# Kernel optimization log

Hardware: AMD Instinct MI355X
Metric: run time of the kernel (lower is better)

## Reference

```python
import jax, jax.numpy as jnp
import numpy as np

P = 4096      # particles per event
F = 128       # max features per particle (inner ragged axis)
H = 128       # hidden_size


def setup_inputs() -> dict:
    key = jax.random.key(0)
    ks = jax.random.split(key, 12)
    s = 1.0 / np.sqrt(H)  # torch RNN default init scale
    u = lambda k, shp: jax.random.uniform(k, shp, jnp.float32, -s, s)
    event = jax.random.normal(ks[0], (P, F, 1), jnp.float32)
    lengths = jnp.maximum(1, jax.random.randint(ks[1], (P,), 0, F))  # ragged lengths in [1, F)
    return {
        "event": event,
        "lengths": lengths,
        "W_ih1": u(ks[2], (H, 1)), "W_hh1": u(ks[3], (H, H)),
        "b_ih1": u(ks[4], (H,)),   "b_hh1": u(ks[5], (H,)),
        "W_ih2": u(ks[6], (H, H)), "W_hh2": u(ks[7], (H, H)),
        "b_ih2": u(ks[8], (H,)),   "b_hh2": u(ks[9], (H,)),
    }


def reference(event, lengths, W_ih1, W_hh1, b_ih1, b_hh1,
              W_ih2, W_hh2, b_ih2, b_hh2):
    # net1: vanilla tanh RNN over each particle's feature sequence (batched over P).
    # Ragged lengths handled by masking the hidden-state update past each length.
    Pn, Fn, _ = event.shape
    mask = jnp.arange(Fn)[:, None] < lengths[None, :]      # [F, P]
    xs = jnp.transpose(event, (1, 0, 2))                   # [F, P, 1] time-major

    def step1(h, xm):
        x, m = xm                                          # x:[P,1], m:[P]
        h_new = jnp.tanh(x @ W_ih1.T + b_ih1 + h @ W_hh1.T + b_hh1)
        return jnp.where(m[:, None], h_new, h), None

    h0 = jnp.zeros((Pn, H), event.dtype)
    h1, _ = jax.lax.scan(step1, h0, (xs, mask))            # final hidden per particle: [P, H]

    # net2: tanh RNN over the sequence of particle hidden states (unbatched).
    def step2(h, x):
        return jnp.tanh(x @ W_ih2.T + b_ih2 + h @ W_hh2.T + b_hh2), None

    h2, _ = jax.lax.scan(step2, jnp.zeros((H,), event.dtype), h1)
    return h2[None, :]                                     # torch hidden shape (1, H)
```

## Files before the change

kernel.cpp:

```cpp
#include <hip/hip_runtime.h>


constexpr int PN = 4096;
constexpr int FN = 128;
constexpr int HN = 128;
constexpr int CH  = 64;
constexpr int NCH = PN / CH;

__device__ __forceinline__ float fast_tanh(float x) {
    float e = __expf(2.0f * x);
    return 1.0f - 2.0f / (e + 1.0f);
}

__device__ __forceinline__ void lds_barrier() {
    asm volatile("s_waitcnt lgkmcnt(0)\n\ts_barrier" ::: "memory");
}

__device__ __forceinline__ float dpp_xor1(float x) {
    return __int_as_float(__builtin_amdgcn_update_dpp(
        0, __float_as_int(x), 0xB1 , 0xF, 0xF, true));
}
__device__ __forceinline__ float dpp_xor2(float x) {
    return __int_as_float(__builtin_amdgcn_update_dpp(
        0, __float_as_int(x), 0x4E , 0xF, 0xF, true));
}
__device__ __forceinline__ float dpp_xor4(float x, bool hi) {
    int a = __builtin_amdgcn_update_dpp(0, __float_as_int(x), 0x104, 0xF, 0xF, true);
    int b = __builtin_amdgcn_update_dpp(0, __float_as_int(x), 0x114, 0xF, 0xF, true);
    return __int_as_float(hi ? b : a);
}
__device__ __forceinline__ float dpp_xor8(float x, bool hi) {
    int a = __builtin_amdgcn_update_dpp(0, __float_as_int(x), 0x108, 0xF, 0xF, true);
    int b = __builtin_amdgcn_update_dpp(0, __float_as_int(x), 0x118, 0xF, 0xF, true);
    return __int_as_float(hi ? b : a);
}

__device__ __forceinline__ float reduce16(const float s[8], int jg) {
    const bool hi8 = (jg & 8) != 0;
    float m0 = hi8 ? s[0] : s[4], k0 = hi8 ? s[4] : s[0];
    float m1 = hi8 ? s[1] : s[5], k1 = hi8 ? s[5] : s[1];
    float m2 = hi8 ? s[2] : s[6], k2 = hi8 ? s[6] : s[2];
    float m3 = hi8 ? s[3] : s[7], k3 = hi8 ? s[7] : s[3];
    float x0 = k0 + dpp_xor8(m0, hi8);
    float x1 = k1 + dpp_xor8(m1, hi8);
    float x2 = k2 + dpp_xor8(m2, hi8);
    float x3 = k3 + dpp_xor8(m3, hi8);
    const bool hi4 = (jg & 4) != 0;
    float y0 = (hi4 ? x2 : x0) + dpp_xor4(hi4 ? x0 : x2, hi4);
    float y1 = (hi4 ? x3 : x1) + dpp_xor4(hi4 ? x1 : x3, hi4);
    const bool hi2 = (jg & 2) != 0;
    float z  = (hi2 ? y1 : y0) + dpp_xor2(hi2 ? y0 : y1);
    z += dpp_xor1(z);
    return z;
}
__device__ __forceinline__ int reduce16_cidx(int jg) {
    return ((jg >> 3) & 1) * 4 + ((jg >> 2) & 1) * 2 + ((jg >> 1) & 1);
}

__global__ __launch_bounds__(256) void net1_kernel(
    const float* __restrict__ event,
    const int*   __restrict__ lengths,
    const float* __restrict__ W_ih1,
    const float* __restrict__ W_hh1,
    const float* __restrict__ b_ih1,
    const float* __restrict__ b_hh1,
    const float* __restrict__ W_ih2,
    const float* __restrict__ b_ih2,
    const float* __restrict__ b_hh2,
    float* __restrict__ U)
{
    const int p    = blockIdx.x;
    const int tid  = threadIdx.x;
    const int wv   = tid >> 6;
    const int lane = tid & 63;
    const int jg   = lane & 15;
    const int og16 = (wv << 2) + (lane >> 4);
    const int rot  = (jg >> 2) & 1;
    const int oi_w = og16 * 8 + reduce16_cidx(jg);

    __shared__ float h[2][HN];
    __shared__ float ev[FN];

    if (tid < FN) ev[tid]   = event[p * FN + tid];
    if (tid < HN) h[0][tid] = 0.0f;

    float w[8][8];
    #pragma unroll
    for (int c = 0; c < 8; ++c) {
        const float* row = W_hh1 + (og16 * 8 + c) * HN + jg * 8;
        #pragma unroll
        for (int t = 0; t < 2; ++t) {
            const int krot = (t + rot) & 1;
            float4 v = *reinterpret_cast<const float4*>(row + 4 * krot);
            w[c][4*t+0] = v.x; w[c][4*t+1] = v.y;
            w[c][4*t+2] = v.z; w[c][4*t+3] = v.w;
        }
    }
    const float wx_own   = W_ih1[oi_w];
    const float bias_own = b_ih1[oi_w] + b_hh1[oi_w];
    const int   len      = lengths[p];

    __syncthreads();

    for (int t = 0; t < len; ++t) {
        const int cur = t & 1;
        const float x = ev[t];

        const float* base = &h[cur][jg * 8];
        float s[8] = {0,0,0,0,0,0,0,0};
        #pragma unroll
        for (int tt = 0; tt < 2; ++tt) {
            const int krot = (tt + rot) & 1;
            float4 hv = *reinterpret_cast<const float4*>(base + 4 * krot);
            #pragma unroll
            for (int c = 0; c < 8; ++c) {
                s[c] = fmaf(w[c][4*tt+0], hv.x, s[c]);
                s[c] = fmaf(w[c][4*tt+1], hv.y, s[c]);
                s[c] = fmaf(w[c][4*tt+2], hv.z, s[c]);
                s[c] = fmaf(w[c][4*tt+3], hv.w, s[c]);
            }
        }
        const float z  = reduce16(s, jg);
        const float hn = fast_tanh(z + fmaf(wx_own, x, bias_own));
        if ((jg & 1) == 0) h[cur ^ 1][oi_w] = hn;
        lds_barrier();
    }

    if (tid < HN) {
        const float4* h4 = reinterpret_cast<const float4*>(h[len & 1]);
        const float4* w2 = reinterpret_cast<const float4*>(W_ih2 + tid * HN);
        float a0 = b_ih2[tid] + b_hh2[tid], a1 = 0.f, a2 = 0.f, a3 = 0.f;
        #pragma unroll
        for (int k = 0; k < HN / 4; ++k) {
            float4 hv = h4[k];
            float4 wv = w2[k];
            a0 = fmaf(wv.x, hv.x, a0);
            a1 = fmaf(wv.y, hv.y, a1);
            a2 = fmaf(wv.z, hv.z, a2);
            a3 = fmaf(wv.w, hv.w, a3);
        }
        U[p * HN + tid] = (a0 + a1) + (a2 + a3);
    }
}

__global__ __launch_bounds__(256) void net2_kernel(
    const float* __restrict__ U,
    const float* __restrict__ W_hh2,
    float* __restrict__ out)
{
    const int tid  = threadIdx.x;
    const int wv   = tid >> 6;
    const int lane = tid & 63;
    const int jg   = lane & 15;
    const int og16 = (wv << 2) + (lane >> 4);
    const int rot  = (jg >> 2) & 1;
    const int oi_w = og16 * 8 + reduce16_cidx(jg);

    __shared__ float h[2][HN];
    __shared__ float Ulds[2][CH * HN];

    float w[8][8];
    #pragma unroll
    for (int c = 0; c < 8; ++c) {
        const float* row = W_hh2 + (og16 * 8 + c) * HN + jg * 8;
        #pragma unroll
        for (int t = 0; t < 2; ++t) {
            const int krot = (t + rot) & 1;
            float4 v = *reinterpret_cast<const float4*>(row + 4 * krot);
            w[c][4*t+0] = v.x; w[c][4*t+1] = v.y;
            w[c][4*t+2] = v.z; w[c][4*t+3] = v.w;
        }
    }

    {
        const float4* g = reinterpret_cast<const float4*>(U);
        float4*       l = reinterpret_cast<float4*>(&Ulds[0][0]);
        #pragma unroll
        for (int r = 0; r < 8; ++r) l[r * 256 + tid] = g[r * 256 + tid];
    }
    if (tid < HN) h[0][tid] = 0.0f;
    __syncthreads();

    int buf = 0;
    for (int c = 0; c < NCH; ++c) {
        const int nb = buf ^ 1;

        float4 st[8];
        const int cg = (c + 1 < NCH) ? (c + 1) : c;
        {
            const float4* gsrc = reinterpret_cast<const float4*>(U + cg * CH * HN);
            #pragma unroll
            for (int r = 0; r < 8; ++r) st[r] = gsrc[r * 256 + tid];
        }

        for (int s2 = 0; s2 < CH; ++s2) {
            const int hc = s2 & 1;
            const float u_cur = Ulds[buf][s2 * HN + oi_w];

            const float* base = &h[hc][jg * 8];
            float s[8] = {0,0,0,0,0,0,0,0};
            #pragma unroll
            for (int tt = 0; tt < 2; ++tt) {
                const int krot = (tt + rot) & 1;
                float4 hv = *reinterpret_cast<const float4*>(base + 4 * krot);
                #pragma unroll
                for (int cc = 0; cc < 8; ++cc) {
                    s[cc] = fmaf(w[cc][4*tt+0], hv.x, s[cc]);
                    s[cc] = fmaf(w[cc][4*tt+1], hv.y, s[cc]);
                    s[cc] = fmaf(w[cc][4*tt+2], hv.z, s[cc]);
                    s[cc] = fmaf(w[cc][4*tt+3], hv.w, s[cc]);
                }
            }
            const float z  = reduce16(s, jg);
            const float hn = fast_tanh(z + u_cur);
            if ((jg & 1) == 0) h[hc ^ 1][oi_w] = hn;
            lds_barrier();
        }

        {
            float4* ldst = reinterpret_cast<float4*>(&Ulds[nb][0]);
            #pragma unroll
            for (int r = 0; r < 8; ++r) ldst[r * 256 + tid] = st[r];
        }
        __syncthreads();
        buf = nb;
    }

    if (tid < HN) out[tid] = h[0][tid];
}

extern "C" void kernel_launch(void* const* d_in, const int* in_sizes, int n_in,
                              void* d_out, int out_size, void* d_ws, size_t ws_size,
                              hipStream_t stream)
{
    const float* event   = (const float*)d_in[0];
    const int*   lengths = (const int*)  d_in[1];
    const float* W_ih1   = (const float*)d_in[2];
    const float* W_hh1   = (const float*)d_in[3];
    const float* b_ih1   = (const float*)d_in[4];
    const float* b_hh1   = (const float*)d_in[5];
    const float* W_ih2   = (const float*)d_in[6];
    const float* W_hh2   = (const float*)d_in[7];
    const float* b_ih2   = (const float*)d_in[8];
    const float* b_hh2   = (const float*)d_in[9];
    float* out = (float*)d_out;
    float* U   = (float*)d_ws;

    hipLaunchKernelGGL(net1_kernel, dim3(PN), dim3(256), 0, stream,
                       event, lengths, W_ih1, W_hh1, b_ih1, b_hh1,
                       W_ih2, b_ih2, b_hh2, U);
    hipLaunchKernelGGL(net2_kernel, dim3(1), dim3(256), 0, stream,
                       U, W_hh2, out);
}
```

Measured before the change: 1.875 ms.

## Add per-chunk readiness counters and shorten net2 reduction to 8-lane groups

```diff
diff --git a/kernel.cpp b/kernel.cpp
--- a/kernel.cpp
+++ b/kernel.cpp
@@ -18,11 +18,11 @@
 
 __device__ __forceinline__ float dpp_xor1(float x) {
     return __int_as_float(__builtin_amdgcn_update_dpp(
-        0, __float_as_int(x), 0xB1 , 0xF, 0xF, true));
+        0, __float_as_int(x), 0xB1, 0xF, 0xF, true));
 }
 __device__ __forceinline__ float dpp_xor2(float x) {
     return __int_as_float(__builtin_amdgcn_update_dpp(
-        0, __float_as_int(x), 0x4E , 0xF, 0xF, true));
+        0, __float_as_int(x), 0x4E, 0xF, 0xF, true));
 }
 __device__ __forceinline__ float dpp_xor4(float x, bool hi) {
     int a = __builtin_amdgcn_update_dpp(0, __float_as_int(x), 0x104, 0xF, 0xF, true);
@@ -57,6 +57,7 @@
     return ((jg >> 3) & 1) * 4 + ((jg >> 2) & 1) * 2 + ((jg >> 1) & 1);
 }
 
+template <bool SYNC>
 __global__ __launch_bounds__(256) void net1_kernel(
     const float* __restrict__ event,
     const int*   __restrict__ lengths,
@@ -67,7 +68,8 @@
     const float* __restrict__ W_ih2,
     const float* __restrict__ b_ih2,
     const float* __restrict__ b_hh2,
-    float* __restrict__ U)
+    float* __restrict__ U,
+    unsigned*   cnt)
 {
     const int p    = blockIdx.x;
     const int tid  = threadIdx.x;
@@ -105,7 +107,6 @@
     for (int t = 0; t < len; ++t) {
         const int cur = t & 1;
         const float x = ev[t];
-
         const float* base = &h[cur][jg * 8];
         float s[8] = {0,0,0,0,0,0,0,0};
         #pragma unroll
@@ -141,37 +142,58 @@
         }
         U[p * HN + tid] = (a0 + a1) + (a2 + a3);
     }
-}
-
+
+    if (SYNC) {
+        __syncthreads();
+        if (tid == 0) {
+            __hip_atomic_fetch_add(&cnt[p >> 6], 1u,
+                                   __ATOMIC_RELEASE, __HIP_MEMORY_SCOPE_AGENT);
+        }
+    }
+}
+
+__device__ __forceinline__ void wait_chunk(const unsigned* cnt, int c) {
+    while (__hip_atomic_load(&cnt[c], __ATOMIC_ACQUIRE,
+                             __HIP_MEMORY_SCOPE_AGENT) < (unsigned)CH) {
+        __builtin_amdgcn_s_sleep(8);
+    }
+}
+
+template <bool SYNC>
 __global__ __launch_bounds__(256) void net2_kernel(
     const float* __restrict__ U,
     const float* __restrict__ W_hh2,
-    float* __restrict__ out)
+    float* __restrict__ out,
+    const unsigned* cnt)
 {
     const int tid  = threadIdx.x;
     const int wv   = tid >> 6;
     const int lane = tid & 63;
-    const int jg   = lane & 15;
-    const int og16 = (wv << 2) + (lane >> 4);
-    const int rot  = (jg >> 2) & 1;
-    const int oi_w = og16 * 8 + reduce16_cidx(jg);
+    const int jg   = lane & 7;
+    const int ogl  = lane >> 3;
+    const int og   = (wv << 3) + ogl;
+    const int rot  = jg >> 1;
+    const bool hi4 = (jg & 4) != 0;
+    const int cidx = ((jg >> 2) & 1) * 2 + ((jg >> 1) & 1);
+    const int oi_w = og * 4 + cidx;
 
     __shared__ float h[2][HN];
     __shared__ float Ulds[2][CH * HN];
 
-    float w[8][8];
+    float w[4][16];
     #pragma unroll
-    for (int c = 0; c < 8; ++c) {
-        const float* row = W_hh2 + (og16 * 8 + c) * HN + jg * 8;
-        #pragma unroll
-        for (int t = 0; t < 2; ++t) {
-            const int krot = (t + rot) & 1;
+    for (int c = 0; c < 4; ++c) {
+        const float* row = W_hh2 + (og * 4 + c) * HN + jg * 16;
+        #pragma unroll
+        for (int t = 0; t < 4; ++t) {
+            const int krot = (t + rot) & 3;
             float4 v = *reinterpret_cast<const float4*>(row + 4 * krot);
             w[c][4*t+0] = v.x; w[c][4*t+1] = v.y;
             w[c][4*t+2] = v.z; w[c][4*t+3] = v.w;
         }
     }
 
+    if (SYNC) wait_chunk(cnt, 0);
     {
         const float4* g = reinterpret_cast<const float4*>(U);
         float4*       l = reinterpret_cast<float4*>(&Ulds[0][0]);
@@ -184,9 +206,11 @@
     int buf = 0;
     for (int c = 0; c < NCH; ++c) {
         const int nb = buf ^ 1;
+        const int cg = (c + 1 < NCH) ? (c + 1) : c;
+
+        if (SYNC) wait_chunk(cnt, cg);
 
         float4 st[8];
-        const int cg = (c + 1 < NCH) ? (c + 1) : c;
         {
             const float4* gsrc = reinterpret_cast<const float4*>(U + cg * CH * HN);
             #pragma unroll
@@ -197,21 +221,32 @@
             const int hc = s2 & 1;
             const float u_cur = Ulds[buf][s2 * HN + oi_w];
 
-            const float* base = &h[hc][jg * 8];
-            float s[8] = {0,0,0,0,0,0,0,0};
-            #pragma unroll
-            for (int tt = 0; tt < 2; ++tt) {
-                const int krot = (tt + rot) & 1;
+            const float* base = &h[hc][jg * 16];
+            float s0 = 0.f, s1 = 0.f, s2a = 0.f, s3 = 0.f;
+            #pragma unroll
+            for (int t = 0; t < 4; ++t) {
+                const int krot = (t + rot) & 3;
                 float4 hv = *reinterpret_cast<const float4*>(base + 4 * krot);
-                #pragma unroll
-                for (int cc = 0; cc < 8; ++cc) {
-                    s[cc] = fmaf(w[cc][4*tt+0], hv.x, s[cc]);
-                    s[cc] = fmaf(w[cc][4*tt+1], hv.y, s[cc]);
-                    s[cc] = fmaf(w[cc][4*tt+2], hv.z, s[cc]);
-                    s[cc] = fmaf(w[cc][4*tt+3], hv.w, s[cc]);
-                }
+                s0  = fmaf(w[0][4*t+0], hv.x, s0);  s0  = fmaf(w[0][4*t+1], hv.y, s0);
+                s0  = fmaf(w[0][4*t+2], hv.z, s0);  s0  = fmaf(w[0][4*t+3], hv.w, s0);
+                s1  = fmaf(w[1][4*t+0], hv.x, s1);  s1  = fmaf(w[1][4*t+1], hv.y, s1);
+                s1  = fmaf(w[1][4*t+2], hv.z, s1);  s1  = fmaf(w[1][4*t+3], hv.w, s1);
+                s2a = fmaf(w[2][4*t+0], hv.x, s2a); s2a = fmaf(w[2][4*t+1], hv.y, s2a);
+                s2a = fmaf(w[2][4*t+2], hv.z, s2a); s2a = fmaf(w[2][4*t+3], hv.w, s2a);
+                s3  = fmaf(w[3][4*t+0], hv.x, s3);  s3  = fmaf(w[3][4*t+1], hv.y, s3);
+                s3  = fmaf(w[3][4*t+2], hv.z, s3);  s3  = fmaf(w[3][4*t+3], hv.w, s3);
             }
-            const float z  = reduce16(s, jg);
+
+            const bool lo4 = !hi4;
+            float t0 = lo4 ? s2a : s0;
+            float t1 = lo4 ? s3  : s1;
+            float x0 = (lo4 ? s0 : s2a) + dpp_xor4(t0, hi4);
+            float x1 = (lo4 ? s1 : s3 ) + dpp_xor4(t1, hi4);
+            const bool lo2 = (jg & 2) == 0;
+            float t2 = lo2 ? x1 : x0;
+            float z  = (lo2 ? x0 : x1) + dpp_xor2(t2);
+            z += dpp_xor1(z);
+
             const float hn = fast_tanh(z + u_cur);
             if ((jg & 1) == 0) h[hc ^ 1][oi_w] = hn;
             lds_barrier();
@@ -245,10 +280,19 @@
     const float* b_hh2   = (const float*)d_in[9];
     float* out = (float*)d_out;
     float* U   = (float*)d_ws;
-
-    hipLaunchKernelGGL(net1_kernel, dim3(PN), dim3(256), 0, stream,
-                       event, lengths, W_ih1, W_hh1, b_ih1, b_hh1,
-                       W_ih2, b_ih2, b_hh2, U);
-    hipLaunchKernelGGL(net2_kernel, dim3(1), dim3(256), 0, stream,
-                       U, W_hh2, out);
-}
+    unsigned* cnt = (unsigned*)(U + (size_t)PN * HN);
+
+    const bool sync_ok =
+        ws_size >= (size_t)PN * HN * sizeof(float) + NCH * sizeof(unsigned);
+
+    if (sync_ok) {
+        hipMemsetAsync(cnt, 0, NCH * sizeof(unsigned), stream);
+        net1_kernel<true><<<dim3(PN), dim3(256), 0, stream>>>(
+            event, lengths, W_ih1, W_hh1, b_ih1, b_hh1, W_ih2, b_ih2, b_hh2, U, cnt);
+        net2_kernel<true><<<dim3(1), dim3(256), 0, stream>>>(U, W_hh2, out, cnt);
+    } else {
+        net1_kernel<false><<<dim3(PN), dim3(256), 0, stream>>>(
+            event, lengths, W_ih1, W_hh1, b_ih1, b_hh1, W_ih2, b_ih2, b_hh2, U, cnt);
+        net2_kernel<false><<<dim3(1), dim3(256), 0, stream>>>(U, W_hh2, out, cnt);
+    }
+}
```

New measurement: 1.763 ms. -5.9%, faster.
